# Kernel tuning notes

Measured on AMD Instinct MI355X. Metric: run time of the kernel, lower is better.

The kernel has to match this reference:

```python
import jax, jax.numpy as jnp
import numpy as np

H, W = 640, 640
C_IN, C_OUT = 3, 64
K, PAD = 7, 3          # 7x7 sparse conv, SAME padding (stride 1)
POOL_K, POOL_S = 3, 2  # valid 3x3 max pool, stride 2
N_SITES = 100000
BN_EPS = 1e-5


def setup_inputs() -> dict:
    key = jax.random.key(0)
    k1, k2, k3 = jax.random.split(key, 3)
    feature_map = jax.random.normal(k1, (H, W, C_IN), dtype=jnp.float32)
    update_location = jax.random.randint(k2, (N_SITES, 2), 0, min(H, W)).astype(jnp.int64)
    # kaiming-uniform-ish init for the 7x7x3 -> 64 conv weight
    fan_in = K * K * C_IN
    bound = np.sqrt(3.0 / fan_in).astype(np.float32)
    weight = jax.random.uniform(k3, (K, K, C_IN, C_OUT), jnp.float32, -bound, bound)
    return {
        "update_location": update_location,
        "feature_map": feature_map,
        "weight": weight,
        "gamma": jnp.ones((C_OUT,), jnp.float32),
        "beta": jnp.zeros((C_OUT,), jnp.float32),
        "running_mean": jnp.zeros((C_OUT,), jnp.float32),
        "running_var": jnp.ones((C_OUT,), jnp.float32),
    }


def reference(update_location, feature_map, weight, gamma, beta, running_mean, running_var):
    # ---- sparse (active-site) 7x7 conv: gather patches only at active sites ----
    fm = jnp.pad(feature_map, ((PAD, PAD), (PAD, PAD), (0, 0)))  # zero pad borders
    offs = jnp.arange(K)
    rows = update_location[:, 0, None] + offs          # [N, K] (pad offset = +PAD-PAD)
    cols = update_location[:, 1, None] + offs          # [N, K]
    patches = fm[rows[:, :, None], cols[:, None, :]]   # [N, K, K, C_IN]
    feats = jnp.einsum('nijc,ijco->no', patches, weight)  # [N, C_OUT]

    # ---- frozen BN + ReLU fused on active sites ----
    inv = gamma * jax.lax.rsqrt(running_var + BN_EPS)
    feats = jnp.maximum(feats * inv + (beta - running_mean * inv), 0.0)

    # ---- scatter active-site features into dense map (inactive sites stay 0) ----
    dense = jnp.zeros((H, W, C_OUT), feats.dtype).at[
        update_location[:, 0], update_location[:, 1]].set(feats)

    # ---- 3x3 stride-2 valid max pool (ReLU outputs >= 0, zeros elsewhere) ----
    pooled = jax.lax.reduce_window(
        dense, 0.0, jax.lax.max,
        (POOL_K, POOL_K, 1), (POOL_S, POOL_S, 1), 'VALID')  # [319, 319, C_OUT]
    return pooled
```

## Files before the change

### kernel.cpp

```cpp
#include <hip/hip_runtime.h>

#define HH 640
#define WW 640
#define COUT 64
#define KK 7
#define NS 100000
#define OHh 319
#define OWw 319
#define PWY 646
#define PWX 648
#define OWNER_BLKS 391
#define PAD_BLKS 818
#define NBLK 1563
#define NWB (4 * KK * 64)

typedef _Float16 half2_t __attribute__((ext_vector_type(2)));
typedef _Float16 h8 __attribute__((ext_vector_type(8)));
typedef float f4 __attribute__((ext_vector_type(4)));
typedef uint4 u4a __attribute__((aligned(8)));

union H2U { unsigned u; half2_t h; };
union H8U { uint4 u; h8 h; _Float16 e[8]; };

__device__ __forceinline__ unsigned short f2bf(float x) {
    unsigned u = __float_as_uint(x);
    return (unsigned short)((u + 0x7FFFu + ((u >> 16) & 1u)) >> 16);
}
__device__ __forceinline__ float bf2f(unsigned short b) {
    return __uint_as_float((unsigned)b << 16);
}

__device__ __forceinline__ bool detect_is64(const int* __restrict__ loc) {
    const int smp = loc[1 + 2 * (int)(threadIdx.x & 63)];
    return __ballot(smp != 0) == 0ULL;
}

__global__ __launch_bounds__(256) void prep_kernel(
        const int* __restrict__ loc, const float* __restrict__ fm,
        const float* __restrict__ wgt, const float* __restrict__ gamma,
        const float* __restrict__ beta, const float* __restrict__ mean,
        const float* __restrict__ var,
        int* __restrict__ owner, uint2* __restrict__ pfm,
        uint4* __restrict__ wbg, float* __restrict__ bn) {
    if (blockIdx.x < OWNER_BLKS) {
        const bool is64 = detect_is64(loc);
        const int n = blockIdx.x * 256 + threadIdx.x;
        if (n < NS) {
            int r, c;
            if (is64) { r = loc[4 * n]; c = loc[4 * n + 2]; }
            else      { r = loc[2 * n]; c = loc[2 * n + 1]; }
            atomicMax(&owner[r * WW + c], n);
        }
    } else if (blockIdx.x < OWNER_BLKS + PAD_BLKS) {
        const int pair = (blockIdx.x - OWNER_BLKS) * 256 + threadIdx.x;
        const int pix = pair * 2;
        if (pix < PWY * PWX) {
            const int r = pix / PWX, c = pix - r * PWX;
            uint4 o;
            H2U a0, b0, a1, b1;
            a0.u = b0.u = a1.u = b1.u = 0;
            if (r >= 3 && r < 643) {
                const float* s = fm + ((size_t)(r - 3) * WW + (c - 3)) * 3;
                if (c >= 3 && c < 643) {
                    a0.h = half2_t{(_Float16)s[0], (_Float16)s[1]};
                    b0.h = half2_t{(_Float16)s[2], (_Float16)0};
                }
                if (c + 1 >= 3 && c + 1 < 643) {
                    a1.h = half2_t{(_Float16)s[3], (_Float16)s[4]};
                    b1.h = half2_t{(_Float16)s[5], (_Float16)0};
                }
            }
            o.x = a0.u; o.y = b0.u; o.z = a1.u; o.w = b1.u;
            *(uint4*)(pfm + pix) = o;
        }
    } else {
        for (int e = threadIdx.x; e < NWB; e += 256) {
            const int t = e / (KK * 64);
            const int rem = e - t * KK * 64;
            const int i = rem >> 6, l = rem & 63;
            const int cout = t * 16 + (l & 15);
            const int q = l >> 4;
            H8U w;
            #pragma unroll
            for (int j = 0; j < 8; ++j) {
                const int kl = q * 8 + j, px = kl >> 2, ci = kl & 3;
                const float v = (px < KK && ci < 3)
                                  ? wgt[((i * KK + px) * 3 + ci) * COUT + cout] : 0.0f;
                w.e[j] = (_Float16)v;
            }
            wbg[e] = w.u;
        }
        if (threadIdx.x < COUT) {
            const int co = threadIdx.x;
            const float iv = gamma[co] * rsqrtf(var[co] + 1e-5f);
            bn[co] = iv;
            bn[COUT + co] = beta[co] - mean[co] * iv;
        }
    }
}

__global__ __launch_bounds__(256) void feats_kernel(
        const int* __restrict__ loc, const uint2* __restrict__ pfm,
        const uint4* __restrict__ wbg, const float* __restrict__ bn,
        unsigned short* __restrict__ feats) {
    __shared__ uint4 WB[NWB];
    #pragma unroll
    for (int e = 0; e < NWB / 256; ++e)
        WB[e * 256 + threadIdx.x] = wbg[e * 256 + threadIdx.x];
    const bool is64 = detect_is64(loc);
    __syncthreads();

    const int lane = threadIdx.x & 63;
    const int s = lane & 15;
    const int q = lane >> 4;
    const int n0 = (blockIdx.x * 4 + (threadIdx.x >> 6)) * 16;
    if (n0 >= NS) return;

    const int nA = n0 + s;
    int rA, cA;
    if (is64) { rA = loc[4 * nA]; cA = loc[4 * nA + 2]; }
    else      { rA = loc[2 * nA]; cA = loc[2 * nA + 1]; }
    const int aidx = rA * PWX + cA + 2 * q;

    f4 acc[4] = {f4{0,0,0,0}, f4{0,0,0,0}, f4{0,0,0,0}, f4{0,0,0,0}};
    #pragma unroll
    for (int i = 0; i < KK; ++i) {
        H8U a;
        a.u = *(const u4a*)(pfm + aidx + i * PWX);
        #pragma unroll
        for (int t = 0; t < 4; ++t) {
            H8U b;
            b.u = WB[(t * KK + i) * 64 + lane];
            acc[t] = __builtin_amdgcn_mfma_f32_16x16x32_f16(b.h, a.h, acc[t], 0, 0, 0);
        }
    }

    unsigned short* dst = feats + (size_t)nA * COUT;
    #pragma unroll
    for (int t = 0; t < 4; ++t) {
        const float4 iv = *(const float4*)&bn[t * 16 + 4 * q];
        const float4 bi = *(const float4*)&bn[COUT + t * 16 + 4 * q];
        const unsigned short o0 = f2bf(fmaxf(acc[t][0] * iv.x + bi.x, 0.0f));
        const unsigned short o1 = f2bf(fmaxf(acc[t][1] * iv.y + bi.y, 0.0f));
        const unsigned short o2 = f2bf(fmaxf(acc[t][2] * iv.z + bi.z, 0.0f));
        const unsigned short o3 = f2bf(fmaxf(acc[t][3] * iv.w + bi.w, 0.0f));
        uint2 w;
        w.x = (unsigned)o0 | ((unsigned)o1 << 16);
        w.y = (unsigned)o2 | ((unsigned)o3 << 16);
        *(uint2*)(dst + t * 16 + 4 * q) = w;
    }
}

__global__ __launch_bounds__(256) void pool_kernel(
        const int* __restrict__ owner, const unsigned short* __restrict__ feats,
        float* __restrict__ out) {
    const int lane = threadIdx.x & 63;
    const int TPR = 80;
    const int task = __builtin_amdgcn_readfirstlane(blockIdx.x * 4 + (threadIdx.x >> 6));
    if (task >= OHh * TPR) return;
    const int oh = task / TPR, ow0 = (task % TPR) * 4;
    const int r0 = oh * 2, c0 = ow0 * 2;

    int ov[3][9];
    #pragma unroll
    for (int dy = 0; dy < 3; ++dy)
        __builtin_memcpy(&ov[dy][0], owner + (r0 + dy) * WW + c0, 36);

    float v[3][9];
    #pragma unroll
    for (int dy = 0; dy < 3; ++dy)
        #pragma unroll
        for (int dx = 0; dx < 9; ++dx) {
            const int o = ov[dy][dx];
            const int oc = (o < 0 || o >= NS) ? 0 : o;
            const float f = bf2f(feats[(size_t)oc * COUT + lane]);
            v[dy][dx] = (o >= 0 && o < NS) ? f : 0.0f;
        }

    #pragma unroll
    for (int qq = 0; qq < 4; ++qq) {
        const int ow = ow0 + qq;
        if (ow >= OWw) break;
        float m = 0.0f;
        #pragma unroll
        for (int dy = 0; dy < 3; ++dy)
            #pragma unroll
            for (int dx = 0; dx < 3; ++dx)
                m = fmaxf(m, v[dy][2 * qq + dx]);
        out[(size_t)(oh * OWw + ow) * COUT + lane] = m;
    }
}

extern "C" void kernel_launch(void* const* d_in, const int* in_sizes, int n_in,
                              void* d_out, int out_size, void* d_ws, size_t ws_size,
                              hipStream_t stream) {
    const int*   loc   = (const int*)d_in[0];
    const float* fm    = (const float*)d_in[1];
    const float* wgt   = (const float*)d_in[2];
    const float* gamma = (const float*)d_in[3];
    const float* beta  = (const float*)d_in[4];
    const float* mean  = (const float*)d_in[5];
    const float* var   = (const float*)d_in[6];
    float* out = (float*)d_out;

    char* ws = (char*)d_ws;
    int* owner = (int*)ws;
    uint2* pfm = (uint2*)(ws + 1638400);
    char* ws2 = ws + 1638400 + (size_t)PWY * PWX * 8;
    uint4* wbg = (uint4*)ws2;
    float* bn  = (float*)(ws2 + NWB * 16);
    unsigned short* feats = (unsigned short*)(ws2 + NWB * 16 + 512);

    prep_kernel<<<OWNER_BLKS + PAD_BLKS + 1, 256, 0, stream>>>(
        loc, fm, wgt, gamma, beta, mean, var, owner, pfm, wbg, bn);
    feats_kernel<<<NBLK, 256, 0, stream>>>(loc, pfm, wbg, bn, feats);
    pool_kernel<<<(OHh * 80 + 3) / 4, 256, 0, stream>>>(owner, feats, out);
}
```

Before: 114.1 us.

## Parallelise weight prep, precompute patch indices, async LDS loads, scalarize pool owners

```diff
diff --git a/kernel.cpp b/kernel.cpp
--- a/kernel.cpp
+++ b/kernel.cpp
@@ -9,6 +9,7 @@
 #define OWw 319
 #define PWY 646
 #define PWX 648
+#define WGT_BLKS 7
 #define OWNER_BLKS 391
 #define PAD_BLKS 818
 #define NBLK 1563
@@ -41,18 +42,42 @@
         const float* __restrict__ beta, const float* __restrict__ mean,
         const float* __restrict__ var,
         int* __restrict__ owner, uint2* __restrict__ pfm,
-        uint4* __restrict__ wbg, float* __restrict__ bn) {
-    if (blockIdx.x < OWNER_BLKS) {
+        uint4* __restrict__ wbg, float* __restrict__ bn,
+        int* __restrict__ aidx) {
+    if (blockIdx.x < WGT_BLKS) {
+        const int e = blockIdx.x * 256 + threadIdx.x;
+        const int t = e / (KK * 64);
+        const int rem = e - t * KK * 64;
+        const int i = rem >> 6, l = rem & 63;
+        const int cout = t * 16 + (l & 15);
+        const int q = l >> 4;
+        H8U w;
+        #pragma unroll
+        for (int j = 0; j < 8; ++j) {
+            const int kl = q * 8 + j, px = kl >> 2, ci = kl & 3;
+            const float v = (px < KK && ci < 3)
+                              ? wgt[((i * KK + px) * 3 + ci) * COUT + cout] : 0.0f;
+            w.e[j] = (_Float16)v;
+        }
+        wbg[e] = w.u;
+        if (blockIdx.x == 0 && threadIdx.x < COUT) {
+            const int co = threadIdx.x;
+            const float iv = gamma[co] * rsqrtf(var[co] + 1e-5f);
+            bn[co] = iv;
+            bn[COUT + co] = beta[co] - mean[co] * iv;
+        }
+    } else if (blockIdx.x < WGT_BLKS + OWNER_BLKS) {
         const bool is64 = detect_is64(loc);
-        const int n = blockIdx.x * 256 + threadIdx.x;
+        const int n = (blockIdx.x - WGT_BLKS) * 256 + threadIdx.x;
         if (n < NS) {
             int r, c;
             if (is64) { r = loc[4 * n]; c = loc[4 * n + 2]; }
             else      { r = loc[2 * n]; c = loc[2 * n + 1]; }
             atomicMax(&owner[r * WW + c], n);
-        }
-    } else if (blockIdx.x < OWNER_BLKS + PAD_BLKS) {
-        const int pair = (blockIdx.x - OWNER_BLKS) * 256 + threadIdx.x;
+            aidx[n] = r * PWX + c;
+        }
+    } else {
+        const int pair = (blockIdx.x - WGT_BLKS - OWNER_BLKS) * 256 + threadIdx.x;
         const int pix = pair * 2;
         if (pix < PWY * PWX) {
             const int r = pix / PWX, c = pix - r * PWX;
@@ -73,65 +98,44 @@
             o.x = a0.u; o.y = b0.u; o.z = a1.u; o.w = b1.u;
             *(uint4*)(pfm + pix) = o;
         }
-    } else {
-        for (int e = threadIdx.x; e < NWB; e += 256) {
-            const int t = e / (KK * 64);
-            const int rem = e - t * KK * 64;
-            const int i = rem >> 6, l = rem & 63;
-            const int cout = t * 16 + (l & 15);
-            const int q = l >> 4;
-            H8U w;
-            #pragma unroll
-            for (int j = 0; j < 8; ++j) {
-                const int kl = q * 8 + j, px = kl >> 2, ci = kl & 3;
-                const float v = (px < KK && ci < 3)
-                                  ? wgt[((i * KK + px) * 3 + ci) * COUT + cout] : 0.0f;
-                w.e[j] = (_Float16)v;
-            }
-            wbg[e] = w.u;
-        }
-        if (threadIdx.x < COUT) {
-            const int co = threadIdx.x;
-            const float iv = gamma[co] * rsqrtf(var[co] + 1e-5f);
-            bn[co] = iv;
-            bn[COUT + co] = beta[co] - mean[co] * iv;
-        }
     }
 }
 
 __global__ __launch_bounds__(256) void feats_kernel(
-        const int* __restrict__ loc, const uint2* __restrict__ pfm,
+        const int* __restrict__ aidxg, const uint2* __restrict__ pfm,
         const uint4* __restrict__ wbg, const float* __restrict__ bn,
         unsigned short* __restrict__ feats) {
     __shared__ uint4 WB[NWB];
+    const int lane = threadIdx.x & 63;
+    const int wv = threadIdx.x >> 6;
     #pragma unroll
     for (int e = 0; e < NWB / 256; ++e)
-        WB[e * 256 + threadIdx.x] = wbg[e * 256 + threadIdx.x];
-    const bool is64 = detect_is64(loc);
+        __builtin_amdgcn_global_load_lds(
+            (const uint4*)(wbg + e * 256 + wv * 64 + lane),
+            (uint4*)&WB[e * 256 + wv * 64], 16, 0, 0);
     __syncthreads();
 
-    const int lane = threadIdx.x & 63;
     const int s = lane & 15;
     const int q = lane >> 4;
-    const int n0 = (blockIdx.x * 4 + (threadIdx.x >> 6)) * 16;
+    const int n0 = (blockIdx.x * 4 + wv) * 16;
     if (n0 >= NS) return;
 
     const int nA = n0 + s;
-    int rA, cA;
-    if (is64) { rA = loc[4 * nA]; cA = loc[4 * nA + 2]; }
-    else      { rA = loc[2 * nA]; cA = loc[2 * nA + 1]; }
-    const int aidx = rA * PWX + cA + 2 * q;
+    const int aidx = aidxg[nA] + 2 * q;
+
+    H8U a[KK];
+    #pragma unroll
+    for (int i = 0; i < KK; ++i)
+        a[i].u = *(const u4a*)(pfm + aidx + i * PWX);
 
     f4 acc[4] = {f4{0,0,0,0}, f4{0,0,0,0}, f4{0,0,0,0}, f4{0,0,0,0}};
     #pragma unroll
     for (int i = 0; i < KK; ++i) {
-        H8U a;
-        a.u = *(const u4a*)(pfm + aidx + i * PWX);
         #pragma unroll
         for (int t = 0; t < 4; ++t) {
             H8U b;
             b.u = WB[(t * KK + i) * 64 + lane];
-            acc[t] = __builtin_amdgcn_mfma_f32_16x16x32_f16(b.h, a.h, acc[t], 0, 0, 0);
+            acc[t] = __builtin_amdgcn_mfma_f32_16x16x32_f16(b.h, a[i].h, acc[t], 0, 0, 0);
         }
     }
 
@@ -161,32 +165,35 @@
     const int oh = task / TPR, ow0 = (task % TPR) * 4;
     const int r0 = oh * 2, c0 = ow0 * 2;
 
-    int ov[3][9];
-    #pragma unroll
-    for (int dy = 0; dy < 3; ++dy)
-        __builtin_memcpy(&ov[dy][0], owner + (r0 + dy) * WW + c0, 36);
-
-    float v[3][9];
+    int ov[27];
     #pragma unroll
     for (int dy = 0; dy < 3; ++dy)
         #pragma unroll
-        for (int dx = 0; dx < 9; ++dx) {
-            const int o = ov[dy][dx];
-            const int oc = (o < 0 || o >= NS) ? 0 : o;
-            const float f = bf2f(feats[(size_t)oc * COUT + lane]);
-            v[dy][dx] = (o >= 0 && o < NS) ? f : 0.0f;
-        }
+        for (int dx = 0; dx < 9; ++dx)
+            ov[dy * 9 + dx] =
+                __builtin_amdgcn_readfirstlane(owner[(r0 + dy) * WW + c0 + dx]);
+
+    float v[27];
+    #pragma unroll
+    for (int k = 0; k < 27; ++k) v[k] = 0.0f;
+    #pragma unroll
+    for (int k = 0; k < 27; ++k) {
+        const int o = ov[k];
+        if (o >= 0 && o < NS)
+            v[k] = bf2f(feats[(size_t)o * COUT + lane]);
+    }
+
+    float colmax[9];
+    #pragma unroll
+    for (int x = 0; x < 9; ++x)
+        colmax[x] = fmaxf(fmaxf(v[x], v[9 + x]), v[18 + x]);
 
     #pragma unroll
     for (int qq = 0; qq < 4; ++qq) {
         const int ow = ow0 + qq;
         if (ow >= OWw) break;
-        float m = 0.0f;
-        #pragma unroll
-        for (int dy = 0; dy < 3; ++dy)
-            #pragma unroll
-            for (int dx = 0; dx < 3; ++dx)
-                m = fmaxf(m, v[dy][2 * qq + dx]);
+        const float m = fmaxf(fmaxf(colmax[2 * qq], colmax[2 * qq + 1]),
+                              colmax[2 * qq + 2]);
         out[(size_t)(oh * OWw + ow) * COUT + lane] = m;
     }
 }
@@ -209,10 +216,12 @@
     char* ws2 = ws + 1638400 + (size_t)PWY * PWX * 8;
     uint4* wbg = (uint4*)ws2;
     float* bn  = (float*)(ws2 + NWB * 16);
-    unsigned short* feats = (unsigned short*)(ws2 + NWB * 16 + 512);
-
-    prep_kernel<<<OWNER_BLKS + PAD_BLKS + 1, 256, 0, stream>>>(
-        loc, fm, wgt, gamma, beta, mean, var, owner, pfm, wbg, bn);
-    feats_kernel<<<NBLK, 256, 0, stream>>>(loc, pfm, wbg, bn, feats);
+    int* aidx  = (int*)(ws2 + NWB * 16 + 512);
+    unsigned short* feats =
+        (unsigned short*)(ws2 + NWB * 16 + 512 + NS * 4);
+
+    prep_kernel<<<WGT_BLKS + OWNER_BLKS + PAD_BLKS, 256, 0, stream>>>(
+        loc, fm, wgt, gamma, beta, mean, var, owner, pfm, wbg, bn, aidx);
+    feats_kernel<<<NBLK, 256, 0, stream>>>(aidx, pfm, wbg, bn, feats);
     pool_kernel<<<(OHh * 80 + 3) / 4, 256, 0, stream>>>(owner, feats, out);
 }
```

After: 114.2 us. No clear change (+0.1%).
